# Optimization experiments

Measured on AMD Instinct MI355X. Metric: run time of the kernel, lower is better.

The kernel has to match this reference:

```python
import jax, jax.numpy as jnp
import numpy as np

NU, NF, E, FIN, H = 50000, 25000, 500000, 128, 128
NEG_SLOPE_ATT = 0.2   # PyG GATConv default negative_slope
NEG_SLOPE_MLP = 0.01  # nn.LeakyReLU default
BN_EPS = 1e-5


def setup_inputs() -> dict:
    key = jax.random.key(0)
    ks = iter(jax.random.split(key, 64))

    def rn(shape, scale=0.05):
        return jax.random.normal(next(ks), shape, dtype=jnp.float32) * scale

    inp = {
        "x_user": jax.random.normal(next(ks), (NU, FIN), dtype=jnp.float32),
        "x_food": jax.random.normal(next(ks), (NF, FIN), dtype=jnp.float32),
        "uf_src": jax.random.randint(next(ks), (E,), 0, NU),
        "uf_dst": jax.random.randint(next(ks), (E,), 0, NF),
        "fu_src": jax.random.randint(next(ks), (E,), 0, NF),
        "fu_dst": jax.random.randint(next(ks), (E,), 0, NU),
        "he_user": jax.random.randint(next(ks), (E,), 0, NU),
        "he_food": jax.random.randint(next(ks), (E,), 0, NF),
        "batch_health_scores": jax.random.uniform(next(ks), (E,), dtype=jnp.float32),
    }
    # GATConv params per layer (1,2) per edge type (uf: user->food, fu: food->user)
    for L, fin in ((1, FIN), (2, H)):
        for et in ("uf", "fu"):
            inp[f"w{L}_{et}_src"] = rn((fin, H))
            inp[f"w{L}_{et}_dst"] = rn((fin, H))
            inp[f"a{L}_{et}_src"] = rn((H,))
            inp[f"a{L}_{et}_dst"] = rn((H,))
            inp[f"b{L}_{et}"] = jnp.zeros((H,), jnp.float32)
    # BatchNorm per layer per node type
    for L in (1, 2):
        for nt in ("user", "food"):
            inp[f"bn{L}_{nt}_g"] = jnp.ones((H,), jnp.float32)
            inp[f"bn{L}_{nt}_b"] = jnp.zeros((H,), jnp.float32)
    # health preference MLP: Linear(H, H//2) -> LeakyReLU -> Linear(H//2, 1) -> Tanh
    inp["hw1"] = rn((H, H // 2)); inp["hb1"] = jnp.zeros((H // 2,), jnp.float32)
    inp["hw2"] = rn((H // 2, 1)); inp["hb2"] = jnp.zeros((1,), jnp.float32)
    return inp


def _gat(x_src, x_dst, src, dst, w_s, w_d, a_s, a_d, b, n_dst):
    """PyG GATConv, heads=1, no self loops, eval (no attention dropout)."""
    hs = x_src @ w_s                      # [Ns, H]
    hd = x_dst @ w_d                      # [Nd, H]
    asn = hs @ a_s                        # per-src-node scalar
    adn = hd @ a_d                        # per-dst-node scalar
    e = jax.nn.leaky_relu(asn[src] + adn[dst], NEG_SLOPE_ATT)  # [E]
    m = jax.ops.segment_max(e, dst, num_segments=n_dst)
    m = jnp.where(jnp.isfinite(m), m, 0.0)
    ee = jnp.exp(e - m[dst])
    den = jax.ops.segment_sum(ee, dst, num_segments=n_dst)
    alpha = ee / (den[dst] + 1e-16)
    out = jax.ops.segment_sum(alpha[:, None] * hs[src], dst, num_segments=n_dst)
    return out + b


def _bn_elu(x, g, b):
    mu = x.mean(0)
    var = x.var(0)  # biased var, as torch BN uses for normalization
    return jax.nn.elu((x - mu) * jax.lax.rsqrt(var + BN_EPS) * g + b)


def reference(x_user, x_food, uf_src, uf_dst, fu_src, fu_dst, he_user, he_food,
              batch_health_scores,
              w1_uf_src, w1_uf_dst, a1_uf_src, a1_uf_dst, b1_uf,
              w1_fu_src, w1_fu_dst, a1_fu_src, a1_fu_dst, b1_fu,
              w2_uf_src, w2_uf_dst, a2_uf_src, a2_uf_dst, b2_uf,
              w2_fu_src, w2_fu_dst, a2_fu_src, a2_fu_dst, b2_fu,
              bn1_user_g, bn1_user_b, bn1_food_g, bn1_food_b,
              bn2_user_g, bn2_user_b, bn2_food_g, bn2_food_b,
              hw1, hb1, hw2, hb2):
    # ---- layer 1 (HeteroConv, sum aggr; each node type has one incoming edge type)
    xf = _gat(x_user, x_food, uf_src, uf_dst, w1_uf_src, w1_uf_dst, a1_uf_src, a1_uf_dst, b1_uf, NF)
    xu = _gat(x_food, x_user, fu_src, fu_dst, w1_fu_src, w1_fu_dst, a1_fu_src, a1_fu_dst, b1_fu, NU)
    xu = _bn_elu(xu, bn1_user_g, bn1_user_b)
    xf = _bn_elu(xf, bn1_food_g, bn1_food_b)
    # ---- layer 2
    xf2 = _gat(xu, xf, uf_src, uf_dst, w2_uf_src, w2_uf_dst, a2_uf_src, a2_uf_dst, b2_uf, NF)
    xu2 = _gat(xf, xu, fu_src, fu_dst, w2_fu_src, w2_fu_dst, a2_fu_src, a2_fu_dst, b2_fu, NU)
    xu2 = _bn_elu(xu2, bn2_user_g, bn2_user_b)
    xf2 = _bn_elu(xf2, bn2_food_g, bn2_food_b)
    # ---- health-score scatter_add update
    h = jax.nn.leaky_relu(xu2 @ hw1 + hb1, NEG_SLOPE_MLP)
    prefs = jnp.tanh(h @ hw2 + hb2)                      # [NU, 1]
    adjusted = prefs[he_user, 0] * batch_health_scores   # [E]
    # expand+scatter_add over rows == broadcast segment_sum of the per-edge scalar
    s = jax.ops.segment_sum(adjusted, he_food, num_segments=NF)  # [NF]
    xf2 = xf2 + 0.1 * s[:, None]
    return (xu2, xf2, prefs)
```

## Files before the change

### kernel.cpp

```cpp
#include <hip/hip_runtime.h>
#include <cstddef>

#define NU_ 50000
#define NF_ 25000
#define E_  500000

typedef __attribute__((ext_vector_type(8))) short short8v;
typedef __attribute__((ext_vector_type(4))) float float4v;

constexpr int LDR = 136;

static __device__ __forceinline__ ushort f2bf(float f) {
    uint u = __float_as_uint(f);
    uint r = (u + 0x7fffu + ((u >> 16) & 1u)) >> 16;
    return (ushort)r;
}
static __device__ __forceinline__ float bf2f(ushort u) {
    return __uint_as_float(((uint)u) << 16);
}

struct PPArgs {
    const float* xu; const float* xf;
    ushort* bu; ushort* bfo;
    const float* W[5];  ushort* T[5];
    const float* waW[8]; const float* waA[8];
    float* vall;
};

__global__ __launch_bounds__(256) void preprocess(PPArgs A) {
    const int nbA = NU_ * 32 / 256;
    const int nbB = NF_ * 32 / 256;
    const int nbC = 4 * 64 + 32;
    int b = blockIdx.x, t = threadIdx.x;
    if (b < nbA) {
        int i = b * 256 + t;
        float4 v = ((const float4*)A.xu)[i];
        ushort4 o; o.x = f2bf(v.x); o.y = f2bf(v.y); o.z = f2bf(v.z); o.w = f2bf(v.w);
        ((ushort4*)A.bu)[i] = o;
    } else if (b < nbA + nbB) {
        int i = (b - nbA) * 256 + t;
        float4 v = ((const float4*)A.xf)[i];
        ushort4 o; o.x = f2bf(v.x); o.y = f2bf(v.y); o.z = f2bf(v.z); o.w = f2bf(v.w);
        ((ushort4*)A.bfo)[i] = o;
    } else if (b < nbA + nbB + nbC) {
        int cb = b - nbA - nbB;
        int m, wb, sh;
        if (cb < 256) { m = cb >> 6; wb = cb & 63; sh = 7; }
        else          { m = 4; wb = cb - 256; sh = 6; }
        int idx = wb * 256 + t;
        int k = idx >> sh, c = idx & ((1 << sh) - 1);
        A.T[m][c * 128 + k] = f2bf(A.W[m][idx]);
    } else {
        int db = b - nbA - nbB - nbC;
        int row = db * 4 + (t >> 6);
        int m = row >> 7, k = row & 127, lane = t & 63;
        float2 w = ((const float2*)(A.waW[m] + k * 128))[lane];
        float2 av = ((const float2*)A.waA[m])[lane];
        float s = w.x * av.x + w.y * av.y;
        #pragma unroll
        for (int o = 32; o; o >>= 1) s += __shfl_xor(s, o);
        if (lane == 0) A.vall[row] = s;
    }
}

__global__ void csr_count_both(const int* __restrict__ uf_dst, const int* __restrict__ fu_dst,
                               int* __restrict__ deg_f, int* __restrict__ deg_u, int EB) {
    int b = blockIdx.x;
    const int* dst; int* deg; int e;
    if (b < EB) { dst = uf_dst; deg = deg_f; e = b * 256 + threadIdx.x; }
    else        { dst = fu_dst; deg = deg_u; e = (b - EB) * 256 + threadIdx.x; }
    if (e < E_) atomicAdd(&deg[dst[e]], 1);
}

__global__ __launch_bounds__(256) void csr_psum_both(const int* __restrict__ deg_f, int* __restrict__ part_f,
                                                     const int* __restrict__ deg_u, int* __restrict__ part_u) {
    const int NBF = (NF_ + 1023) / 1024;
    __shared__ int wsum[4];
    int b = blockIdx.x;
    const int* deg; int* part; int N, bb;
    if (b < NBF) { deg = deg_f; part = part_f; N = NF_; bb = b; }
    else         { deg = deg_u; part = part_u; N = NU_; bb = b - NBF; }
    int base = bb * 1024;
    int s = 0;
    for (int i = threadIdx.x; i < 1024; i += 256) {
        int idx = base + i;
        if (idx < N) s += deg[idx];
    }
    #pragma unroll
    for (int o = 32; o; o >>= 1) s += __shfl_xor(s, o);
    if ((threadIdx.x & 63) == 0) wsum[threadIdx.x >> 6] = s;
    __syncthreads();
    if (threadIdx.x == 0) part[bb] = wsum[0] + wsum[1] + wsum[2] + wsum[3];
}

__global__ __launch_bounds__(128) void csr_scan_both(int* __restrict__ part_f, int* __restrict__ offN_f,
                                                     int* __restrict__ part_u, int* __restrict__ offN_u) {
    int w = threadIdx.x >> 6, lane = threadIdx.x & 63;
    int nb; int* part; int* offN;
    if (w == 0) { nb = (NF_ + 1023) / 1024; part = part_f; offN = offN_f; }
    else        { nb = (NU_ + 1023) / 1024; part = part_u; offN = offN_u; }
    int v = (lane < nb) ? part[lane] : 0;
    int incl = v;
    #pragma unroll
    for (int o = 1; o < 64; o <<= 1) {
        int t = __shfl_up(incl, o);
        if (lane >= o) incl += t;
    }
    if (lane < nb) part[lane] = incl - v;
    if (lane == 63) *offN = incl;
}

__global__ __launch_bounds__(256) void csr_bscan_both(const int* __restrict__ deg_f, const int* __restrict__ part_f,
                                                      int* __restrict__ uf_off, int* __restrict__ cur_f,
                                                      const int* __restrict__ deg_u, const int* __restrict__ part_u,
                                                      int* __restrict__ fu_off, int* __restrict__ cur_u) {
    const int NBF = (NF_ + 1023) / 1024;
    __shared__ int wsum[4];
    int blk = blockIdx.x;
    const int *deg, *part; int *off, *cursor; int N, bb;
    if (blk < NBF) { deg = deg_f; part = part_f; off = uf_off; cursor = cur_f; N = NF_; bb = blk; }
    else           { deg = deg_u; part = part_u; off = fu_off; cursor = cur_u; N = NU_; bb = blk - NBF; }
    int t = threadIdx.x;
    int lane = t & 63, w = t >> 6;
    int base = bb * 1024 + t * 4;
    int l0 = 0, l1 = 0, l2 = 0, l3 = 0;
    if (base + 3 < N) {
        int4 v = *(const int4*)(deg + base);
        l0 = v.x; l1 = v.y; l2 = v.z; l3 = v.w;
    } else {
        if (base + 0 < N) l0 = deg[base + 0];
        if (base + 1 < N) l1 = deg[base + 1];
        if (base + 2 < N) l2 = deg[base + 2];
    }
    int tsum = l0 + l1 + l2 + l3;
    int incl = tsum;
    #pragma unroll
    for (int o = 1; o < 64; o <<= 1) {
        int tt = __shfl_up(incl, o);
        if (lane >= o) incl += tt;
    }
    int lexcl = incl - tsum;
    if (lane == 63) wsum[w] = incl;
    __syncthreads();
    int p = part[bb] + lexcl;
    for (int i = 0; i < w; ++i) p += wsum[i];
    if (base + 0 < N) { off[base + 0] = p; cursor[base + 0] = p; } p += l0;
    if (base + 1 < N) { off[base + 1] = p; cursor[base + 1] = p; } p += l1;
    if (base + 2 < N) { off[base + 2] = p; cursor[base + 2] = p; } p += l2;
    if (base + 3 < N) { off[base + 3] = p; cursor[base + 3] = p; }
}

__global__ void csr_fill_both(const int* __restrict__ uf_src, const int* __restrict__ uf_dst,
                              int* __restrict__ cur_f, int* __restrict__ uf_esrc,
                              const int* __restrict__ fu_src, const int* __restrict__ fu_dst,
                              int* __restrict__ cur_u, int* __restrict__ fu_esrc, int EB) {
    int b = blockIdx.x;
    const int *src, *dst; int *cursor, *esrc; int e;
    if (b < EB) { src = uf_src; dst = uf_dst; cursor = cur_f; esrc = uf_esrc; e = b * 256 + threadIdx.x; }
    else        { src = fu_src; dst = fu_dst; cursor = cur_u; esrc = fu_esrc; e = (b - EB) * 256 + threadIdx.x; }
    if (e >= E_) return;
    int p = atomicAdd(&cursor[dst[e]], 1);
    esrc[p] = src[e];
}

static __device__ __forceinline__ void gemm_tile(const ushort* __restrict__ Xb,
                                                 const ushort* __restrict__ Wt,
                                                 ushort* __restrict__ C, int N, int row0,
                                                 short* Xs, short* Ws) {
    const int t = threadIdx.x;
    for (int i = t; i < 128 * 16; i += 256) {
        int r = i >> 4, c8 = (i & 15) << 3;
        short8v v = {};
        if (row0 + r < N) v = *(const short8v*)(Xb + (size_t)(row0 + r) * 128 + c8);
        *(short8v*)(&Xs[r * LDR + c8]) = v;
    }
    for (int i = t; i < 128 * 16; i += 256) {
        int r = i >> 4, c8 = (i & 15) << 3;
        *(short8v*)(&Ws[r * LDR + c8]) = *(const short8v*)(Wt + r * 128 + c8);
    }
    __syncthreads();

    const int w = t >> 6, l = t & 63;
    const int m0 = (w & 1) * 64;
    const int n0 = (w >> 1) * 64;
    const int frow = l & 15;
    const int koff = (l >> 4) << 3;

    float4v acc[4][4];
    #pragma unroll
    for (int m = 0; m < 4; ++m)
        #pragma unroll
        for (int n = 0; n < 4; ++n) acc[m][n] = (float4v)0.f;

    #pragma unroll
    for (int ks = 0; ks < 4; ++ks) {
        const int k0 = ks * 32 + koff;
        short8v a[4], b[4];
        #pragma unroll
        for (int m = 0; m < 4; ++m)
            a[m] = *(const short8v*)(&Xs[(m0 + m * 16 + frow) * LDR + k0]);
        #pragma unroll
        for (int n = 0; n < 4; ++n)
            b[n] = *(const short8v*)(&Ws[(n0 + n * 16 + frow) * LDR + k0]);
        #pragma unroll
        for (int m = 0; m < 4; ++m)
            #pragma unroll
            for (int n = 0; n < 4; ++n)
                acc[m][n] = __builtin_amdgcn_mfma_f32_16x16x32_bf16(a[m], b[n], acc[m][n], 0, 0, 0);
    }

    const int crow = (l >> 4) << 2;
    const int ccol = l & 15;
    #pragma unroll
    for (int m = 0; m < 4; ++m) {
        #pragma unroll
        for (int r4 = 0; r4 < 4; ++r4) {
            int grow = row0 + m0 + m * 16 + crow + r4;
            if (grow < N) {
                #pragma unroll
                for (int n = 0; n < 4; ++n)
                    C[(size_t)grow * 128 + n0 + n * 16 + ccol] = f2bf(acc[m][n][r4]);
            }
        }
    }
}

__global__ __launch_bounds__(256) void gemm_both(const ushort* __restrict__ Xu, const ushort* __restrict__ Wtu,
                                                 ushort* __restrict__ Cu,
                                                 const ushort* __restrict__ Xf, const ushort* __restrict__ Wtf,
                                                 ushort* __restrict__ Cf) {
    __shared__ short Xs[128 * LDR];
    __shared__ short Ws[128 * LDR];
    const int GU = (NU_ + 127) / 128;
    if ((int)blockIdx.x < GU)
        gemm_tile(Xu, Wtu, Cu, NU_, blockIdx.x * 128, Xs, Ws);
    else
        gemm_tile(Xf, Wtf, Cf, NF_, (blockIdx.x - GU) * 128, Xs, Ws);
}

__global__ __launch_bounds__(256) void matvec4(const ushort* __restrict__ bu, const ushort* __restrict__ bfo,
                                               const float* __restrict__ v_asn_u, const float* __restrict__ v_adn_u,
                                               const float* __restrict__ v_adn_f, const float* __restrict__ v_asn_f,
                                               float* __restrict__ asn_u, float* __restrict__ adn_u,
                                               float* __restrict__ adn_f, float* __restrict__ asn_f) {
    int row = blockIdx.x * 4 + (threadIdx.x >> 6);
    int lane = threadIdx.x & 63;
    const ushort* X; const float *va, *vb; float *oa, *ob; int r;
    if (row < NU_) { X = bu; va = v_asn_u; vb = v_adn_u; oa = asn_u; ob = adn_u; r = row; }
    else {
        r = row - NU_;
        if (r >= NF_) return;
        X = bfo; va = v_adn_f; vb = v_asn_f; oa = adn_f; ob = asn_f;
    }
    ushort2 x = ((const ushort2*)(X + (size_t)r * 128))[lane];
    float2 va2 = ((const float2*)va)[lane];
    float2 vb2 = ((const float2*)vb)[lane];
    float fx = bf2f(x.x), fy = bf2f(x.y);
    float s1 = fx * va2.x + fy * va2.y;
    float s2 = fx * vb2.x + fy * vb2.y;
    #pragma unroll
    for (int o = 32; o; o >>= 1) { s1 += __shfl_xor(s1, o); s2 += __shfl_xor(s2, o); }
    if (lane == 0) { oa[r] = s1; ob[r] = s2; }
}

__global__ __launch_bounds__(256) void gat_agg_both(
        const int* __restrict__ uf_off, const int* __restrict__ uf_esrc,
        const float* __restrict__ asn_u, const float* __restrict__ adn_f,
        const ushort* __restrict__ hs_u, ushort* __restrict__ out_f,
        const int* __restrict__ fu_off, const int* __restrict__ fu_esrc,
        const float* __restrict__ asn_f, const float* __restrict__ adn_u,
        const ushort* __restrict__ hs_f, ushort* __restrict__ out_u) {
    const int NBAF = (NF_ + 3) / 4;
    int blk = blockIdx.x;
    const int *off, *esrc; const float *asn, *adn; const ushort* hs; ushort* out; int Nd, d;
    if (blk < NBAF) {
        off = uf_off; esrc = uf_esrc; asn = asn_u; adn = adn_f; hs = hs_u; out = out_f;
        Nd = NF_; d = blk * 4 + (threadIdx.x >> 6);
    } else {
        off = fu_off; esrc = fu_esrc; asn = asn_f; adn = adn_u; hs = hs_f; out = out_u;
        Nd = NU_; d = (blk - NBAF) * 4 + (threadIdx.x >> 6);
    }
    int lane = threadIdx.x & 63;
    if (d >= Nd) return;
    const int beg = off[d], end = off[d + 1];
    const float ad = adn[d];
    const int qw = lane >> 4, l16 = lane & 15;
    float acc[8] = {0.f, 0.f, 0.f, 0.f, 0.f, 0.f, 0.f, 0.f};
    float den = 0.f;
    for (int base = beg; base < end; base += 64) {
        int e = base + lane;
        int s = 0; float ev = 0.f;
        if (e < end) {
            s = esrc[e];
            float v = asn[s] + ad;
            v = v > 0.f ? v : 0.2f * v;
            ev = __expf(v);
        }
        float r = ev;
        #pragma unroll
        for (int o = 32; o; o >>= 1) r += __shfl_xor(r, o);
        den += r;
        int cnt4 = (min(64, end - base) + 3) & ~3;
        for (int j = 0; j < cnt4; j += 8) {
            int jj = j + qw;
            float ev0 = __shfl(ev, jj);
            int   sj0 = __shfl(s, jj);
            short8v h0 = *(const short8v*)(hs + (size_t)sj0 * 128 + l16 * 8);
            if (j + 4 < cnt4) {
                float ev1 = __shfl(ev, jj + 4);
                int   sj1 = __shfl(s, jj + 4);
                short8v h1 = *(const short8v*)(hs + (size_t)sj1 * 128 + l16 * 8);
                #pragma unroll
                for (int k = 0; k < 8; ++k)
                    acc[k] += ev0 * bf2f((ushort)h0[k]) + ev1 * bf2f((ushort)h1[k]);
            } else {
                #pragma unroll
                for (int k = 0; k < 8; ++k)
                    acc[k] += ev0 * bf2f((ushort)h0[k]);
            }
        }
    }
    #pragma unroll
    for (int k = 0; k < 8; ++k) {
        acc[k] += __shfl_xor(acc[k], 16);
        acc[k] += __shfl_xor(acc[k], 32);
    }
    if (qw == 0) {
        float inv = 1.f / (den + 1e-16f);
        short8v o;
        #pragma unroll
        for (int k = 0; k < 8; ++k) o[k] = (short)f2bf(acc[k] * inv);
        *(short8v*)(out + (size_t)d * 128 + l16 * 8) = o;
    }
}

__global__ __launch_bounds__(256) void bn_stats2b(const ushort* __restrict__ x1, float* __restrict__ stat1,
                                                  int N1, int B1,
                                                  const ushort* __restrict__ x2, float* __restrict__ stat2,
                                                  int N2, int B2) {
    const ushort* x; float* stat; int N, b, nb;
    if ((int)blockIdx.x < B1) { x = x1; stat = stat1; N = N1; b = blockIdx.x; nb = B1; }
    else { x = x2; stat = stat2; N = N2; b = blockIdx.x - B1; nb = B2; }
    const int t = threadIdx.x;
    const int rg = t >> 4;
    const int c16 = t & 15;
    float s[8] = {0,0,0,0,0,0,0,0}, q[8] = {0,0,0,0,0,0,0,0};
    for (int r = b * 16 + rg; r < N; r += nb * 16) {
        short8v v = *(const short8v*)(x + (size_t)r * 128 + c16 * 8);
        #pragma unroll
        for (int k = 0; k < 8; ++k) {
            float f = bf2f((ushort)v[k]);
            s[k] += f; q[k] += f * f;
        }
    }
    #pragma unroll
    for (int k = 0; k < 8; ++k) {
        s[k] += __shfl_xor(s[k], 16); q[k] += __shfl_xor(q[k], 16);
        s[k] += __shfl_xor(s[k], 32); q[k] += __shfl_xor(q[k], 32);
    }
    __shared__ float rs[4][128], rq[4][128];
    const int w = t >> 6, l = t & 63;
    if (l < 16) {
        #pragma unroll
        for (int k = 0; k < 8; ++k) {
            rs[w][l * 8 + k] = s[k];
            rq[w][l * 8 + k] = q[k];
        }
    }
    __syncthreads();
    if (t < 128) {
        float ts = rs[0][t] + rs[1][t] + rs[2][t] + rs[3][t];
        float tq = rq[0][t] + rq[1][t] + rq[2][t] + rq[3][t];
        atomicAdd(&stat[t], ts);
        atomicAdd(&stat[128 + t], tq);
    }
}

__global__ __launch_bounds__(256) void bn_finalize2(float* __restrict__ s1, int N1,
                                                    const float* __restrict__ g1, const float* __restrict__ b1,
                                                    float* __restrict__ s2, int N2,
                                                    const float* __restrict__ g2, const float* __restrict__ b2) {
    int t = threadIdx.x;
    float* s; int N; const float *g, *b; int c;
    if (t < 128) { s = s1; N = N1; g = g1; b = b1; c = t; }
    else         { s = s2; N = N2; g = g2; b = b2; c = t - 128; }
    float invN = 1.0f / N;
    float mu  = s[c] * invN;
    float var = s[128 + c] * invN - mu * mu;
    float sc  = g[c] * rsqrtf(var + 1e-5f);
    s[c]       = sc;
    s[128 + c] = b[c] - mu * sc;
}

__global__ void bn_apply2b(const ushort* __restrict__ x1, const float* __restrict__ ss1,
                           float* __restrict__ xo1, ushort* __restrict__ xb1, int N1,
                           const ushort* __restrict__ x2, const float* __restrict__ ss2,
                           float* __restrict__ xo2, ushort* __restrict__ xb2, int N2) {
    int i = blockIdx.x * 256 + threadIdx.x;
    const ushort* x; const float* ss; float* xo; ushort* xb;
    if (i < N1 * 16) { x = x1; ss = ss1; xo = xo1; xb = xb1; }
    else {
        i -= N1 * 16;
        if (i >= N2 * 16) return;
        x = x2; ss = ss2; xo = xo2; xb = xb2;
    }
    int c16 = i & 15;
    short8v v = *(const short8v*)(x + (size_t)i * 8);
    float sc[8], sh[8];
    *(float4*)&sc[0] = *(const float4*)(ss + c16 * 8);
    *(float4*)&sc[4] = *(const float4*)(ss + c16 * 8 + 4);
    *(float4*)&sh[0] = *(const float4*)(ss + 128 + c16 * 8);
    *(float4*)&sh[4] = *(const float4*)(ss + 128 + c16 * 8 + 4);
    float o[8];
    #pragma unroll
    for (int k = 0; k < 8; ++k) {
        float f = bf2f((ushort)v[k]) * sc[k] + sh[k];
        o[k] = f > 0.f ? f : __expf(f) - 1.f;
    }
    if (xo) {
        *(float4*)(xo + (size_t)i * 8)     = make_float4(o[0], o[1], o[2], o[3]);
        *(float4*)(xo + (size_t)i * 8 + 4) = make_float4(o[4], o[5], o[6], o[7]);
    }
    if (xb) {
        short8v u;
        #pragma unroll
        for (int k = 0; k < 8; ++k) u[k] = (short)f2bf(o[k]);
        *(short8v*)(xb + (size_t)i * 8) = u;
    }
}

__global__ __launch_bounds__(256) void mlp_mfma(const ushort* __restrict__ Xb,
                                                const ushort* __restrict__ Wt,
                                                const float* __restrict__ hb1,
                                                const float* __restrict__ hw2,
                                                const float* __restrict__ hb2,
                                                float* __restrict__ prefs, int N) {
    __shared__ short Xs[128 * LDR];
    __shared__ short Ws[64 * LDR];
    const int t = threadIdx.x;
    const int row0 = blockIdx.x * 128;

    for (int i = t; i < 128 * 16; i += 256) {
        int r = i >> 4, c8 = (i & 15) << 3;
        short8v v = {};
        if (row0 + r < N) v = *(const short8v*)(Xb + (size_t)(row0 + r) * 128 + c8);
        *(short8v*)(&Xs[r * LDR + c8]) = v;
    }
    for (int i = t; i < 64 * 16; i += 256) {
        int r = i >> 4, c8 = (i & 15) << 3;
        *(short8v*)(&Ws[r * LDR + c8]) = *(const short8v*)(Wt + r * 128 + c8);
    }
    __syncthreads();

    const int w = t >> 6, l = t & 63;
    const int m0 = w * 32;
    const int frow = l & 15;
    const int koff = (l >> 4) << 3;

    float4v acc[2][4];
    #pragma unroll
    for (int m = 0; m < 2; ++m)
        #pragma unroll
        for (int n = 0; n < 4; ++n) acc[m][n] = (float4v)0.f;

    #pragma unroll
    for (int ks = 0; ks < 4; ++ks) {
        const int k0 = ks * 32 + koff;
        short8v a[2], b[4];
        #pragma unroll
        for (int m = 0; m < 2; ++m)
            a[m] = *(const short8v*)(&Xs[(m0 + m * 16 + frow) * LDR + k0]);
        #pragma unroll
        for (int n = 0; n < 4; ++n)
            b[n] = *(const short8v*)(&Ws[(n * 16 + frow) * LDR + k0]);
        #pragma unroll
        for (int m = 0; m < 2; ++m)
            #pragma unroll
            for (int n = 0; n < 4; ++n)
                acc[m][n] = __builtin_amdgcn_mfma_f32_16x16x32_bf16(a[m], b[n], acc[m][n], 0, 0, 0);
    }

    float hb1v[4], hw2v[4];
    #pragma unroll
    for (int n = 0; n < 4; ++n) {
        int col = n * 16 + (l & 15);
        hb1v[n] = hb1[col];
        hw2v[n] = hw2[col];
    }
    const float hb2v = hb2[0];
    #pragma unroll
    for (int m = 0; m < 2; ++m) {
        #pragma unroll
        for (int r4 = 0; r4 < 4; ++r4) {
            float p = 0.f;
            #pragma unroll
            for (int n = 0; n < 4; ++n) {
                float v = acc[m][n][r4] + hb1v[n];
                v = v > 0.f ? v : 0.01f * v;
                p += v * hw2v[n];
            }
            p += __shfl_xor(p, 1);
            p += __shfl_xor(p, 2);
            p += __shfl_xor(p, 4);
            p += __shfl_xor(p, 8);
            int grow = row0 + m0 + m * 16 + ((l >> 4) << 2) + r4;
            if ((l & 15) == 0 && grow < N) prefs[grow] = tanhf(p + hb2v);
        }
    }
}

__global__ void health_scatter(const int* __restrict__ hu, const int* __restrict__ hf,
                               const float* __restrict__ score, const float* __restrict__ prefs,
                               float* __restrict__ s, int E) {
    int e = blockIdx.x * 256 + threadIdx.x;
    if (e >= E) return;
    atomicAdd(&s[hf[e]], prefs[hu[e]] * score[e]);
}

__global__ void add_health(float* __restrict__ xf2, const float* __restrict__ s, int n4) {
    int i = blockIdx.x * 256 + threadIdx.x;
    if (i >= n4) return;
    float sv = 0.1f * s[i >> 5];
    float4 v = ((float4*)xf2)[i];
    v.x += sv; v.y += sv; v.z += sv; v.w += sv;
    ((float4*)xf2)[i] = v;
}

extern "C" void kernel_launch(void* const* d_in, const int* in_sizes, int n_in,
                              void* d_out, int out_size, void* d_ws, size_t ws_size,
                              hipStream_t stream) {
    const float* x_user = (const float*)d_in[0];
    const float* x_food = (const float*)d_in[1];
    const int* uf_src = (const int*)d_in[2];
    const int* uf_dst = (const int*)d_in[3];
    const int* fu_src = (const int*)d_in[4];
    const int* fu_dst = (const int*)d_in[5];
    const int* he_user = (const int*)d_in[6];
    const int* he_food = (const int*)d_in[7];
    const float* scores = (const float*)d_in[8];
    const float* bn1_user_g = (const float*)d_in[29];
    const float* bn1_user_b = (const float*)d_in[30];
    const float* bn1_food_g = (const float*)d_in[31];
    const float* bn1_food_b = (const float*)d_in[32];
    const float* bn2_user_g = (const float*)d_in[33];
    const float* bn2_user_b = (const float*)d_in[34];
    const float* bn2_food_g = (const float*)d_in[35];
    const float* bn2_food_b = (const float*)d_in[36];
    const float* hw1 = (const float*)d_in[37];
    const float* hb1 = (const float*)d_in[38];
    const float* hw2 = (const float*)d_in[39];
    const float* hb2 = (const float*)d_in[40];

    float* outp  = (float*)d_out;
    float* xu2   = outp;
    float* xf2   = outp + (size_t)NU_ * 128;
    float* prefs = xf2 + (size_t)NF_ * 128;

    float* ws = (float*)d_ws;
    ushort* hs_u = (ushort*)ws;
    ushort* hs_f = hs_u + (size_t)NU_ * 128;
    float* base1 = ws + (size_t)(NU_ + NF_) * 64;
    ushort* xu1b = (ushort*)base1;
    ushort* xf1b = xu1b + (size_t)NU_ * 128;
    float* base2 = base1 + (size_t)(NU_ + NF_) * 64;
    ushort* xu2b = (ushort*)base2;
    ushort* xf2b = xu2b + (size_t)NU_ * 128;
    float* base3 = base2 + (size_t)(NU_ + NF_) * 64;
    float* asn_u = base3;
    float* adn_u = asn_u + NU_;
    float* asn_f = adn_u + NU_;
    float* adn_f = asn_f + NF_;
    float* stat4 = adn_f + NF_;
    float* sbuf  = stat4 + 1024;
    int*   deg_f = (int*)(sbuf + NF_);
    int*   deg_u = deg_f + NF_;
    int* part_f  = deg_u + NU_;
    int* part_u  = part_f + 32;
    int* uf_off  = part_u + 64;
    int* fu_off  = uf_off + (NF_ + 4);
    int* cur_f   = fu_off + (NU_ + 4);
    int* cur_u   = cur_f + NF_;
    int* uf_esrc = cur_u + NU_;
    int* fu_esrc = uf_esrc + E_;
    ushort* wt0  = (ushort*)(fu_esrc + E_);
    ushort* wt1  = wt0 + 16384;
    ushort* wt2  = wt1 + 16384;
    ushort* wt3  = wt2 + 16384;
    ushort* hw1t = wt3 + 16384;
    float* vall  = (float*)(hw1t + 8192);

    const size_t zero_elems = 1024 + NF_ + NF_ + NU_;
    hipMemsetAsync(stat4, 0, zero_elems * sizeof(float), stream);

    PPArgs pp;
    pp.xu = x_user; pp.xf = x_food; pp.bu = xu2b; pp.bfo = xf2b;
    pp.W[0] = (const float*)d_in[9];  pp.T[0] = wt0;
    pp.W[1] = (const float*)d_in[14]; pp.T[1] = wt1;
    pp.W[2] = (const float*)d_in[19]; pp.T[2] = wt2;
    pp.W[3] = (const float*)d_in[24]; pp.T[3] = wt3;
    pp.W[4] = hw1;                    pp.T[4] = hw1t;
    pp.waW[0] = (const float*)d_in[9];  pp.waA[0] = (const float*)d_in[11];
    pp.waW[1] = (const float*)d_in[10]; pp.waA[1] = (const float*)d_in[12];
    pp.waW[2] = (const float*)d_in[14]; pp.waA[2] = (const float*)d_in[16];
    pp.waW[3] = (const float*)d_in[15]; pp.waA[3] = (const float*)d_in[17];
    pp.waW[4] = (const float*)d_in[19]; pp.waA[4] = (const float*)d_in[21];
    pp.waW[5] = (const float*)d_in[20]; pp.waA[5] = (const float*)d_in[22];
    pp.waW[6] = (const float*)d_in[24]; pp.waA[6] = (const float*)d_in[26];
    pp.waW[7] = (const float*)d_in[25]; pp.waA[7] = (const float*)d_in[27];
    pp.vall = vall;
    const int PPB = NU_ * 32 / 256 + NF_ * 32 / 256 + 288 + 256;
    preprocess<<<PPB, 256, 0, stream>>>(pp);

    const int EB = (E_ + 255) / 256;
    const int NBF = (NF_ + 1023) / 1024;
    const int NBU = (NU_ + 1023) / 1024;
    csr_count_both<<<2 * EB, 256, 0, stream>>>(uf_dst, fu_dst, deg_f, deg_u, EB);
    csr_psum_both<<<NBF + NBU, 256, 0, stream>>>(deg_f, part_f, deg_u, part_u);
    csr_scan_both<<<1, 128, 0, stream>>>(part_f, &uf_off[NF_], part_u, &fu_off[NU_]);
    csr_bscan_both<<<NBF + NBU, 256, 0, stream>>>(deg_f, part_f, uf_off, cur_f,
                                                  deg_u, part_u, fu_off, cur_u);
    csr_fill_both<<<2 * EB, 256, 0, stream>>>(uf_src, uf_dst, cur_f, uf_esrc,
                                              fu_src, fu_dst, cur_u, fu_esrc, EB);

    const int GB   = (NU_ + 127) / 128 + (NF_ + 127) / 128;
    const int MVB  = (NU_ + NF_ + 3) / 4;
    const int AGB  = (NF_ + 3) / 4 + (NU_ + 3) / 4;
    const int APB  = ((NU_ + NF_) * 16 + 255) / 256;

    gemm_both<<<GB, 256, 0, stream>>>(xu2b, wt0, hs_u, xf2b, wt1, hs_f);
    matvec4<<<MVB, 256, 0, stream>>>(xu2b, xf2b, vall + 0, vall + 384, vall + 128, vall + 256,
                                     asn_u, adn_u, adn_f, asn_f);
    gat_agg_both<<<AGB, 256, 0, stream>>>(uf_off, uf_esrc, asn_u, adn_f, hs_u, xf1b,
                                          fu_off, fu_esrc, asn_f, adn_u, hs_f, xu1b);
    bn_stats2b<<<768, 256, 0, stream>>>(xu1b, stat4 + 0, NU_, 512, xf1b, stat4 + 256, NF_, 256);
    bn_finalize2<<<1, 256, 0, stream>>>(stat4 + 0, NU_, bn1_user_g, bn1_user_b,
                                        stat4 + 256, NF_, bn1_food_g, bn1_food_b);
    bn_apply2b<<<APB, 256, 0, stream>>>(xu1b, stat4 + 0,   (float*)nullptr, xu1b, NU_,
                                        xf1b, stat4 + 256, (float*)nullptr, xf1b, NF_);

    gemm_both<<<GB, 256, 0, stream>>>(xu1b, wt2, hs_u, xf1b, wt3, hs_f);
    matvec4<<<MVB, 256, 0, stream>>>(xu1b, xf1b, vall + 512, vall + 896, vall + 640, vall + 768,
                                     asn_u, adn_u, adn_f, asn_f);
    gat_agg_both<<<AGB, 256, 0, stream>>>(uf_off, uf_esrc, asn_u, adn_f, hs_u, xf2b,
                                          fu_off, fu_esrc, asn_f, adn_u, hs_f, xu2b);
    bn_stats2b<<<768, 256, 0, stream>>>(xu2b, stat4 + 512, NU_, 512, xf2b, stat4 + 768, NF_, 256);
    bn_finalize2<<<1, 256, 0, stream>>>(stat4 + 512, NU_, bn2_user_g, bn2_user_b,
                                        stat4 + 768, NF_, bn2_food_g, bn2_food_b);
    bn_apply2b<<<APB, 256, 0, stream>>>(xu2b, stat4 + 512, xu2, xu2b, NU_,
                                        xf2b, stat4 + 768, xf2, (ushort*)nullptr, NF_);

    mlp_mfma<<<(NU_ + 127) / 128, 256, 0, stream>>>(xu2b, hw1t, hb1, hw2, hb2, prefs, NU_);
    health_scatter<<<EB, 256, 0, stream>>>(he_user, he_food, scores, prefs, sbuf, E_);
    add_health<<<(NF_ * 32 + 255) / 256, 256, 0, stream>>>(xf2, sbuf, NF_ * 32);
}
```

Before: 368.4 us.

## Fuse CSR build, matvec, and BN finalize into fewer launches

Folds the degree count into the preprocess kernel, recording each edge's per-destination rank so the fill pass can write without cursor atomics. The partial-sum and scan kernels are merged through a last-block ticket, and BN finalize is merged into the stats kernel the same way. Matvec blocks are appended to the GEMM launch, and the final health-score add is folded into the food BN apply. The goal is fewer kernel launches and less atomic traffic, at the cost of extra rank arrays and ticket-based cross-block synchronization.

```diff
diff --git a/kernel.cpp b/kernel.cpp
--- a/kernel.cpp
+++ b/kernel.cpp
@@ -25,12 +25,17 @@
     const float* W[5];  ushort* T[5];
     const float* waW[8]; const float* waA[8];
     float* vall;
+    const int* uf_dst; const int* fu_dst;
+    int* deg_f; int* deg_u;
+    int* rank_f; int* rank_u;
 };
 
 __global__ __launch_bounds__(256) void preprocess(PPArgs A) {
     const int nbA = NU_ * 32 / 256;
     const int nbB = NF_ * 32 / 256;
     const int nbC = 4 * 64 + 32;
+    const int nbD = 256;
+    const int EB  = (E_ + 255) / 256;
     int b = blockIdx.x, t = threadIdx.x;
     if (b < nbA) {
         int i = b * 256 + t;
@@ -50,7 +55,7 @@
         int idx = wb * 256 + t;
         int k = idx >> sh, c = idx & ((1 << sh) - 1);
         A.T[m][c * 128 + k] = f2bf(A.W[m][idx]);
-    } else {
+    } else if (b < nbA + nbB + nbC + nbD) {
         int db = b - nbA - nbB - nbC;
         int row = db * 4 + (t >> 6);
         int m = row >> 7, k = row & 127, lane = t & 63;
@@ -60,66 +65,71 @@
         #pragma unroll
         for (int o = 32; o; o >>= 1) s += __shfl_xor(s, o);
         if (lane == 0) A.vall[row] = s;
-    }
-}
-
-__global__ void csr_count_both(const int* __restrict__ uf_dst, const int* __restrict__ fu_dst,
-                               int* __restrict__ deg_f, int* __restrict__ deg_u, int EB) {
-    int b = blockIdx.x;
-    const int* dst; int* deg; int e;
-    if (b < EB) { dst = uf_dst; deg = deg_f; e = b * 256 + threadIdx.x; }
-    else        { dst = fu_dst; deg = deg_u; e = (b - EB) * 256 + threadIdx.x; }
-    if (e < E_) atomicAdd(&deg[dst[e]], 1);
-}
-
-__global__ __launch_bounds__(256) void csr_psum_both(const int* __restrict__ deg_f, int* __restrict__ part_f,
-                                                     const int* __restrict__ deg_u, int* __restrict__ part_u) {
+    } else {
+        int cb = b - nbA - nbB - nbC - nbD;
+        const int* dst; int* deg; int* rank; int e;
+        if (cb < EB) { dst = A.uf_dst; deg = A.deg_f; rank = A.rank_f; e = cb * 256 + t; }
+        else         { dst = A.fu_dst; deg = A.deg_u; rank = A.rank_u; e = (cb - EB) * 256 + t; }
+        if (e < E_) rank[e] = atomicAdd(&deg[dst[e]], 1);
+    }
+}
+
+__global__ __launch_bounds__(256) void csr_psum_scan(const int* __restrict__ deg_f, int* __restrict__ part_f,
+                                                     int* __restrict__ offN_f,
+                                                     const int* __restrict__ deg_u, int* __restrict__ part_u,
+                                                     int* __restrict__ offN_u, int* __restrict__ ticket) {
     const int NBF = (NF_ + 1023) / 1024;
+    const int NBU = (NU_ + 1023) / 1024;
     __shared__ int wsum[4];
-    int b = blockIdx.x;
+    __shared__ int sh_last;
+    int b = blockIdx.x, t = threadIdx.x;
     const int* deg; int* part; int N, bb;
     if (b < NBF) { deg = deg_f; part = part_f; N = NF_; bb = b; }
     else         { deg = deg_u; part = part_u; N = NU_; bb = b - NBF; }
     int base = bb * 1024;
     int s = 0;
-    for (int i = threadIdx.x; i < 1024; i += 256) {
+    for (int i = t; i < 1024; i += 256) {
         int idx = base + i;
         if (idx < N) s += deg[idx];
     }
     #pragma unroll
     for (int o = 32; o; o >>= 1) s += __shfl_xor(s, o);
-    if ((threadIdx.x & 63) == 0) wsum[threadIdx.x >> 6] = s;
-    __syncthreads();
-    if (threadIdx.x == 0) part[bb] = wsum[0] + wsum[1] + wsum[2] + wsum[3];
-}
-
-__global__ __launch_bounds__(128) void csr_scan_both(int* __restrict__ part_f, int* __restrict__ offN_f,
-                                                     int* __restrict__ part_u, int* __restrict__ offN_u) {
-    int w = threadIdx.x >> 6, lane = threadIdx.x & 63;
-    int nb; int* part; int* offN;
-    if (w == 0) { nb = (NF_ + 1023) / 1024; part = part_f; offN = offN_f; }
-    else        { nb = (NU_ + 1023) / 1024; part = part_u; offN = offN_u; }
-    int v = (lane < nb) ? part[lane] : 0;
+    if ((t & 63) == 0) wsum[t >> 6] = s;
+    __syncthreads();
+    if (t == 0) {
+        __hip_atomic_store(&part[bb], wsum[0] + wsum[1] + wsum[2] + wsum[3],
+                           __ATOMIC_RELAXED, __HIP_MEMORY_SCOPE_AGENT);
+        __threadfence();
+        sh_last = (atomicAdd(ticket, 1) == NBF + NBU - 1);
+    }
+    __syncthreads();
+    if (!sh_last) return;
+    int w = t >> 6, lane = t & 63;
+    if (w >= 2) return;
+    int nb = w ? NBU : NBF;
+    int* p = w ? part_u : part_f;
+    int* offN = w ? offN_u : offN_f;
+    int v = (lane < nb) ? __hip_atomic_load(&p[lane], __ATOMIC_RELAXED, __HIP_MEMORY_SCOPE_AGENT) : 0;
     int incl = v;
     #pragma unroll
     for (int o = 1; o < 64; o <<= 1) {
-        int t = __shfl_up(incl, o);
-        if (lane >= o) incl += t;
-    }
-    if (lane < nb) part[lane] = incl - v;
+        int tt = __shfl_up(incl, o);
+        if (lane >= o) incl += tt;
+    }
+    if (lane < nb) p[lane] = incl - v;
     if (lane == 63) *offN = incl;
 }
 
 __global__ __launch_bounds__(256) void csr_bscan_both(const int* __restrict__ deg_f, const int* __restrict__ part_f,
-                                                      int* __restrict__ uf_off, int* __restrict__ cur_f,
+                                                      int* __restrict__ uf_off,
                                                       const int* __restrict__ deg_u, const int* __restrict__ part_u,
-                                                      int* __restrict__ fu_off, int* __restrict__ cur_u) {
+                                                      int* __restrict__ fu_off) {
     const int NBF = (NF_ + 1023) / 1024;
     __shared__ int wsum[4];
     int blk = blockIdx.x;
-    const int *deg, *part; int *off, *cursor; int N, bb;
-    if (blk < NBF) { deg = deg_f; part = part_f; off = uf_off; cursor = cur_f; N = NF_; bb = blk; }
-    else           { deg = deg_u; part = part_u; off = fu_off; cursor = cur_u; N = NU_; bb = blk - NBF; }
+    const int *deg, *part; int *off; int N, bb;
+    if (blk < NBF) { deg = deg_f; part = part_f; off = uf_off; N = NF_; bb = blk; }
+    else           { deg = deg_u; part = part_u; off = fu_off; N = NU_; bb = blk - NBF; }
     int t = threadIdx.x;
     int lane = t & 63, w = t >> 6;
     int base = bb * 1024 + t * 4;
@@ -144,23 +154,24 @@
     __syncthreads();
     int p = part[bb] + lexcl;
     for (int i = 0; i < w; ++i) p += wsum[i];
-    if (base + 0 < N) { off[base + 0] = p; cursor[base + 0] = p; } p += l0;
-    if (base + 1 < N) { off[base + 1] = p; cursor[base + 1] = p; } p += l1;
-    if (base + 2 < N) { off[base + 2] = p; cursor[base + 2] = p; } p += l2;
-    if (base + 3 < N) { off[base + 3] = p; cursor[base + 3] = p; }
-}
-
-__global__ void csr_fill_both(const int* __restrict__ uf_src, const int* __restrict__ uf_dst,
-                              int* __restrict__ cur_f, int* __restrict__ uf_esrc,
-                              const int* __restrict__ fu_src, const int* __restrict__ fu_dst,
-                              int* __restrict__ cur_u, int* __restrict__ fu_esrc, int EB) {
+    if (base + 0 < N) off[base + 0] = p; p += l0;
+    if (base + 1 < N) off[base + 1] = p; p += l1;
+    if (base + 2 < N) off[base + 2] = p; p += l2;
+    if (base + 3 < N) off[base + 3] = p;
+}
+
+__global__ void csr_fill2(const int* __restrict__ uf_src, const int* __restrict__ uf_dst,
+                          const int* __restrict__ rank_f, const int* __restrict__ uf_off,
+                          int* __restrict__ uf_esrc,
+                          const int* __restrict__ fu_src, const int* __restrict__ fu_dst,
+                          const int* __restrict__ rank_u, const int* __restrict__ fu_off,
+                          int* __restrict__ fu_esrc, int EB) {
     int b = blockIdx.x;
-    const int *src, *dst; int *cursor, *esrc; int e;
-    if (b < EB) { src = uf_src; dst = uf_dst; cursor = cur_f; esrc = uf_esrc; e = b * 256 + threadIdx.x; }
-    else        { src = fu_src; dst = fu_dst; cursor = cur_u; esrc = fu_esrc; e = (b - EB) * 256 + threadIdx.x; }
+    const int *src, *dst, *rank, *off; int* esrc; int e;
+    if (b < EB) { src = uf_src; dst = uf_dst; rank = rank_f; off = uf_off; esrc = uf_esrc; e = b * 256 + threadIdx.x; }
+    else        { src = fu_src; dst = fu_dst; rank = rank_u; off = fu_off; esrc = fu_esrc; e = (b - EB) * 256 + threadIdx.x; }
     if (e >= E_) return;
-    int p = atomicAdd(&cursor[dst[e]], 1);
-    esrc[p] = src[e];
+    esrc[off[dst[e]] + rank[e]] = src[e];
 }
 
 static __device__ __forceinline__ void gemm_tile(const ushort* __restrict__ Xb,
@@ -225,32 +236,28 @@
     }
 }
 
-__global__ __launch_bounds__(256) void gemm_both(const ushort* __restrict__ Xu, const ushort* __restrict__ Wtu,
-                                                 ushort* __restrict__ Cu,
-                                                 const ushort* __restrict__ Xf, const ushort* __restrict__ Wtf,
-                                                 ushort* __restrict__ Cf) {
+__global__ __launch_bounds__(256) void gemm_mv_both(
+        const ushort* __restrict__ Xu, const ushort* __restrict__ Wtu, ushort* __restrict__ Cu,
+        const ushort* __restrict__ Xf, const ushort* __restrict__ Wtf, ushort* __restrict__ Cf,
+        const float* __restrict__ v_asn_u, const float* __restrict__ v_adn_u,
+        const float* __restrict__ v_adn_f, const float* __restrict__ v_asn_f,
+        float* __restrict__ asn_u, float* __restrict__ adn_u,
+        float* __restrict__ adn_f, float* __restrict__ asn_f) {
     __shared__ short Xs[128 * LDR];
     __shared__ short Ws[128 * LDR];
     const int GU = (NU_ + 127) / 128;
-    if ((int)blockIdx.x < GU)
-        gemm_tile(Xu, Wtu, Cu, NU_, blockIdx.x * 128, Xs, Ws);
-    else
-        gemm_tile(Xf, Wtf, Cf, NF_, (blockIdx.x - GU) * 128, Xs, Ws);
-}
-
-__global__ __launch_bounds__(256) void matvec4(const ushort* __restrict__ bu, const ushort* __restrict__ bfo,
-                                               const float* __restrict__ v_asn_u, const float* __restrict__ v_adn_u,
-                                               const float* __restrict__ v_adn_f, const float* __restrict__ v_asn_f,
-                                               float* __restrict__ asn_u, float* __restrict__ adn_u,
-                                               float* __restrict__ adn_f, float* __restrict__ asn_f) {
-    int row = blockIdx.x * 4 + (threadIdx.x >> 6);
+    const int GF = (NF_ + 127) / 128;
+    int b = blockIdx.x;
+    if (b < GU) { gemm_tile(Xu, Wtu, Cu, NU_, b * 128, Xs, Ws); return; }
+    if (b < GU + GF) { gemm_tile(Xf, Wtf, Cf, NF_, (b - GU) * 128, Xs, Ws); return; }
+    int row = (b - GU - GF) * 4 + (threadIdx.x >> 6);
     int lane = threadIdx.x & 63;
     const ushort* X; const float *va, *vb; float *oa, *ob; int r;
-    if (row < NU_) { X = bu; va = v_asn_u; vb = v_adn_u; oa = asn_u; ob = adn_u; r = row; }
+    if (row < NU_) { X = Xu; va = v_asn_u; vb = v_adn_u; oa = asn_u; ob = adn_u; r = row; }
     else {
         r = row - NU_;
         if (r >= NF_) return;
-        X = bfo; va = v_adn_f; vb = v_asn_f; oa = adn_f; ob = asn_f;
+        X = Xf; va = v_adn_f; vb = v_asn_f; oa = adn_f; ob = asn_f;
     }
     ushort2 x = ((const ushort2*)(X + (size_t)r * 128))[lane];
     float2 va2 = ((const float2*)va)[lane];
@@ -334,10 +341,13 @@
     }
 }
 
-__global__ __launch_bounds__(256) void bn_stats2b(const ushort* __restrict__ x1, float* __restrict__ stat1,
-                                                  int N1, int B1,
-                                                  const ushort* __restrict__ x2, float* __restrict__ stat2,
-                                                  int N2, int B2) {
+__global__ __launch_bounds__(256) void bn_stats_fin(const ushort* __restrict__ x1, float* __restrict__ stat1,
+                                                    int N1, int B1,
+                                                    const float* __restrict__ g1, const float* __restrict__ b1,
+                                                    const ushort* __restrict__ x2, float* __restrict__ stat2,
+                                                    int N2, int B2,
+                                                    const float* __restrict__ g2, const float* __restrict__ b2,
+                                                    int* __restrict__ ticket) {
     const ushort* x; float* stat; int N, b, nb;
     if ((int)blockIdx.x < B1) { x = x1; stat = stat1; N = N1; b = blockIdx.x; nb = B1; }
     else { x = x2; stat = stat2; N = N2; b = blockIdx.x - B1; nb = B2; }
@@ -359,6 +369,7 @@
         s[k] += __shfl_xor(s[k], 32); q[k] += __shfl_xor(q[k], 32);
     }
     __shared__ float rs[4][128], rq[4][128];
+    __shared__ int sh_last;
     const int w = t >> 6, l = t & 63;
     if (l < 16) {
         #pragma unroll
@@ -369,27 +380,25 @@
     }
     __syncthreads();
     if (t < 128) {
-        float ts = rs[0][t] + rs[1][t] + rs[2][t] + rs[3][t];
-        float tq = rq[0][t] + rq[1][t] + rq[2][t] + rq[3][t];
-        atomicAdd(&stat[t], ts);
-        atomicAdd(&stat[128 + t], tq);
-    }
-}
-
-__global__ __launch_bounds__(256) void bn_finalize2(float* __restrict__ s1, int N1,
-                                                    const float* __restrict__ g1, const float* __restrict__ b1,
-                                                    float* __restrict__ s2, int N2,
-                                                    const float* __restrict__ g2, const float* __restrict__ b2) {
-    int t = threadIdx.x;
-    float* s; int N; const float *g, *b; int c;
-    if (t < 128) { s = s1; N = N1; g = g1; b = b1; c = t; }
-    else         { s = s2; N = N2; g = g2; b = b2; c = t - 128; }
-    float invN = 1.0f / N;
-    float mu  = s[c] * invN;
-    float var = s[128 + c] * invN - mu * mu;
+        atomicAdd(&stat[t],       rs[0][t] + rs[1][t] + rs[2][t] + rs[3][t]);
+        atomicAdd(&stat[128 + t], rq[0][t] + rq[1][t] + rq[2][t] + rq[3][t]);
+    }
+    __threadfence();
+    __syncthreads();
+    if (t == 0) sh_last = (atomicAdd(ticket, 1) == B1 + B2 - 1);
+    __syncthreads();
+    if (!sh_last) return;
+    float* sp; int Nn; const float *g, *bb; int c;
+    if (t < 128) { sp = stat1; Nn = N1; g = g1; bb = b1; c = t; }
+    else         { sp = stat2; Nn = N2; g = g2; bb = b2; c = t - 128; }
+    float sum = __hip_atomic_load(&sp[c],       __ATOMIC_RELAXED, __HIP_MEMORY_SCOPE_AGENT);
+    float sq  = __hip_atomic_load(&sp[128 + c], __ATOMIC_RELAXED, __HIP_MEMORY_SCOPE_AGENT);
+    float invN = 1.0f / Nn;
+    float mu  = sum * invN;
+    float var = sq * invN - mu * mu;
     float sc  = g[c] * rsqrtf(var + 1e-5f);
-    s[c]       = sc;
-    s[128 + c] = b[c] - mu * sc;
+    sp[c]       = sc;
+    sp[128 + c] = bb[c] - mu * sc;
 }
 
 __global__ void bn_apply2b(const ushort* __restrict__ x1, const float* __restrict__ ss1,
@@ -416,6 +425,37 @@
     for (int k = 0; k < 8; ++k) {
         float f = bf2f((ushort)v[k]) * sc[k] + sh[k];
         o[k] = f > 0.f ? f : __expf(f) - 1.f;
+    }
+    if (xo) {
+        *(float4*)(xo + (size_t)i * 8)     = make_float4(o[0], o[1], o[2], o[3]);
+        *(float4*)(xo + (size_t)i * 8 + 4) = make_float4(o[4], o[5], o[6], o[7]);
+    }
+    if (xb) {
+        short8v u;
+        #pragma unroll
+        for (int k = 0; k < 8; ++k) u[k] = (short)f2bf(o[k]);
+        *(short8v*)(xb + (size_t)i * 8) = u;
+    }
+}
+
+__global__ void bn_apply1b(const ushort* __restrict__ x, const float* __restrict__ ss,
+                           float* __restrict__ xo, ushort* __restrict__ xb, int N,
+                           const float* __restrict__ health) {
+    int i = blockIdx.x * 256 + threadIdx.x;
+    if (i >= N * 16) return;
+    int c16 = i & 15;
+    short8v v = *(const short8v*)(x + (size_t)i * 8);
+    float sc[8], sh[8];
+    *(float4*)&sc[0] = *(const float4*)(ss + c16 * 8);
+    *(float4*)&sc[4] = *(const float4*)(ss + c16 * 8 + 4);
+    *(float4*)&sh[0] = *(const float4*)(ss + 128 + c16 * 8);
+    *(float4*)&sh[4] = *(const float4*)(ss + 128 + c16 * 8 + 4);
+    float hv = health ? 0.1f * health[i >> 4] : 0.f;
+    float o[8];
+    #pragma unroll
+    for (int k = 0; k < 8; ++k) {
+        float f = bf2f((ushort)v[k]) * sc[k] + sh[k];
+        o[k] = (f > 0.f ? f : __expf(f) - 1.f) + hv;
     }
     if (xo) {
         *(float4*)(xo + (size_t)i * 8)     = make_float4(o[0], o[1], o[2], o[3]);
@@ -515,15 +555,6 @@
     int e = blockIdx.x * 256 + threadIdx.x;
     if (e >= E) return;
     atomicAdd(&s[hf[e]], prefs[hu[e]] * score[e]);
-}
-
-__global__ void add_health(float* __restrict__ xf2, const float* __restrict__ s, int n4) {
-    int i = blockIdx.x * 256 + threadIdx.x;
-    if (i >= n4) return;
-    float sv = 0.1f * s[i >> 5];
-    float4 v = ((float4*)xf2)[i];
-    v.x += sv; v.y += sv; v.z += sv; v.w += sv;
-    ((float4*)xf2)[i] = v;
 }
 
 extern "C" void kernel_launch(void* const* d_in, const int* in_sizes, int n_in,
@@ -574,13 +605,14 @@
     float* sbuf  = stat4 + 1024;
     int*   deg_f = (int*)(sbuf + NF_);
     int*   deg_u = deg_f + NF_;
-    int* part_f  = deg_u + NU_;
+    int*   ticket = deg_u + NU_;
+    int* part_f  = ticket + 4;
     int* part_u  = part_f + 32;
     int* uf_off  = part_u + 64;
     int* fu_off  = uf_off + (NF_ + 4);
-    int* cur_f   = fu_off + (NU_ + 4);
-    int* cur_u   = cur_f + NF_;
-    int* uf_esrc = cur_u + NU_;
+    int* rank_f  = fu_off + (NU_ + 4);
+    int* rank_u  = rank_f + E_;
+    int* uf_esrc = rank_u + E_;
     int* fu_esrc = uf_esrc + E_;
     ushort* wt0  = (ushort*)(fu_esrc + E_);
     ushort* wt1  = wt0 + 16384;
@@ -589,9 +621,10 @@
     ushort* hw1t = wt3 + 16384;
     float* vall  = (float*)(hw1t + 8192);
 
-    const size_t zero_elems = 1024 + NF_ + NF_ + NU_;
+    const size_t zero_elems = 1024 + NF_ + NF_ + NU_ + 4;
     hipMemsetAsync(stat4, 0, zero_elems * sizeof(float), stream);
 
+    const int EB = (E_ + 255) / 256;
     PPArgs pp;
     pp.xu = x_user; pp.xf = x_food; pp.bu = xu2b; pp.bfo = xf2b;
     pp.W[0] = (const float*)d_in[9];  pp.T[0] = wt0;
@@ -608,48 +641,49 @@
     pp.waW[6] = (const float*)d_in[24]; pp.waA[6] = (const float*)d_in[26];
     pp.waW[7] = (const float*)d_in[25]; pp.waA[7] = (const float*)d_in[27];
     pp.vall = vall;
-    const int PPB = NU_ * 32 / 256 + NF_ * 32 / 256 + 288 + 256;
+    pp.uf_dst = uf_dst; pp.fu_dst = fu_dst;
+    pp.deg_f = deg_f; pp.deg_u = deg_u;
+    pp.rank_f = rank_f; pp.rank_u = rank_u;
+    const int PPB = NU_ * 32 / 256 + NF_ * 32 / 256 + 288 + 256 + 2 * EB;
     preprocess<<<PPB, 256, 0, stream>>>(pp);
 
-    const int EB = (E_ + 255) / 256;
     const int NBF = (NF_ + 1023) / 1024;
     const int NBU = (NU_ + 1023) / 1024;
-    csr_count_both<<<2 * EB, 256, 0, stream>>>(uf_dst, fu_dst, deg_f, deg_u, EB);
-    csr_psum_both<<<NBF + NBU, 256, 0, stream>>>(deg_f, part_f, deg_u, part_u);
-    csr_scan_both<<<1, 128, 0, stream>>>(part_f, &uf_off[NF_], part_u, &fu_off[NU_]);
-    csr_bscan_both<<<NBF + NBU, 256, 0, stream>>>(deg_f, part_f, uf_off, cur_f,
-                                                  deg_u, part_u, fu_off, cur_u);
-    csr_fill_both<<<2 * EB, 256, 0, stream>>>(uf_src, uf_dst, cur_f, uf_esrc,
-                                              fu_src, fu_dst, cur_u, fu_esrc, EB);
-
-    const int GB   = (NU_ + 127) / 128 + (NF_ + 127) / 128;
-    const int MVB  = (NU_ + NF_ + 3) / 4;
-    const int AGB  = (NF_ + 3) / 4 + (NU_ + 3) / 4;
-    const int APB  = ((NU_ + NF_) * 16 + 255) / 256;
-
-    gemm_both<<<GB, 256, 0, stream>>>(xu2b, wt0, hs_u, xf2b, wt1, hs_f);
-    matvec4<<<MVB, 256, 0, stream>>>(xu2b, xf2b, vall + 0, vall + 384, vall + 128, vall + 256,
-                                     asn_u, adn_u, adn_f, asn_f);
+    csr_psum_scan<<<NBF + NBU, 256, 0, stream>>>(deg_f, part_f, &uf_off[NF_],
+                                                 deg_u, part_u, &fu_off[NU_], ticket);
+    csr_bscan_both<<<NBF + NBU, 256, 0, stream>>>(deg_f, part_f, uf_off,
+                                                  deg_u, part_u, fu_off);
+    csr_fill2<<<2 * EB, 256, 0, stream>>>(uf_src, uf_dst, rank_f, uf_off, uf_esrc,
+                                          fu_src, fu_dst, rank_u, fu_off, fu_esrc, EB);
+
+    const int GB  = (NU_ + 127) / 128 + (NF_ + 127) / 128;
+    const int MVB = (NU_ + NF_ + 3) / 4;
+    const int AGB = (NF_ + 3) / 4 + (NU_ + 3) / 4;
+    const int APB = ((NU_ + NF_) * 16 + 255) / 256;
+
+    gemm_mv_both<<<GB + MVB, 256, 0, stream>>>(xu2b, wt0, hs_u, xf2b, wt1, hs_f,
+                                               vall + 0, vall + 384, vall + 128, vall + 256,
+                                               asn_u, adn_u, adn_f, asn_f);
     gat_agg_both<<<AGB, 256, 0, stream>>>(uf_off, uf_esrc, asn_u, adn_f, hs_u, xf1b,
                                           fu_off, fu_esrc, asn_f, adn_u, hs_f, xu1b);
-    bn_stats2b<<<768, 256, 0, stream>>>(xu1b, stat4 + 0, NU_, 512, xf1b, stat4 + 256, NF_, 256);
-    bn_finalize2<<<1, 256, 0, stream>>>(stat4 + 0, NU_, bn1_user_g, bn1_user_b,
-                                        stat4 + 256, NF_, bn1_food_g, bn1_food_b);
+    bn_stats_fin<<<768, 256, 0, stream>>>(xu1b, stat4 + 0, NU_, 512, bn1_user_g, bn1_user_b,
+                                          xf1b, stat4 + 256, NF_, 256, bn1_food_g, bn1_food_b,
+                                          ticket + 1);
     bn_apply2b<<<APB, 256, 0, stream>>>(xu1b, stat4 + 0,   (float*)nullptr, xu1b, NU_,
                                         xf1b, stat4 + 256, (float*)nullptr, xf1b, NF_);
 
-    gemm_both<<<GB, 256, 0, stream>>>(xu1b, wt2, hs_u, xf1b, wt3, hs_f);
-    matvec4<<<MVB, 256, 0, stream>>>(xu1b, xf1b, vall + 512, vall + 896, vall + 640, vall + 768,
-                                     asn_u, adn_u, adn_f, asn_f);
+    gemm_mv_both<<<GB + MVB, 256, 0, stream>>>(xu1b, wt2, hs_u, xf1b, wt3, hs_f,
+                                               vall + 512, vall + 896, vall + 640, vall + 768,
+                                               asn_u, adn_u, adn_f, asn_f);
     gat_agg_both<<<AGB, 256, 0, stream>>>(uf_off, uf_esrc, asn_u, adn_f, hs_u, xf2b,
                                           fu_off, fu_esrc, asn_f, adn_u, hs_f, xu2b);
-    bn_stats2b<<<768, 256, 0, stream>>>(xu2b, stat4 + 512, NU_, 512, xf2b, stat4 + 768, NF_, 256);
-    bn_finalize2<<<1, 256, 0, stream>>>(stat4 + 512, NU_, bn2_user_g, bn2_user_b,
-                                        stat4 + 768, NF_, bn2_food_g, bn2_food_b);
-    bn_apply2b<<<APB, 256, 0, stream>>>(xu2b, stat4 + 512, xu2, xu2b, NU_,
-                                        xf2b, stat4 + 768, xf2, (ushort*)nullptr, NF_);
-
+    bn_stats_fin<<<768, 256, 0, stream>>>(xu2b, stat4 + 512, NU_, 512, bn2_user_g, bn2_user_b,
+                                          xf2b, stat4 + 768, NF_, 256, bn2_food_g, bn2_food_b,
+                                          ticket + 2);
+    bn_apply1b<<<(NU_ * 16 + 255) / 256, 256, 0, stream>>>(xu2b, stat4 + 512, xu2, xu2b, NU_,
+                                                           (const float*)nullptr);
     mlp_mfma<<<(NU_ + 127) / 128, 256, 0, stream>>>(xu2b, hw1t, hb1, hw2, hb2, prefs, NU_);
     health_scatter<<<EB, 256, 0, stream>>>(he_user, he_food, scores, prefs, sbuf, E_);
-    add_health<<<(NF_ * 32 + 255) / 256, 256, 0, stream>>>(xf2, sbuf, NF_ * 32);
-}
+    bn_apply1b<<<(NF_ * 16 + 255) / 256, 256, 0, stream>>>(xf2b, stat4 + 768, xf2,
+                                                           (ushort*)nullptr, NF_, sbuf);
+}
```

New measurement: 427.9 us. +16.2%, slower.
